# Kernel optimization log

Hardware: AMD Instinct MI355X
Metric: run time of the kernel (lower is better)

The kernel has to match this reference:

```python
import jax, jax.numpy as jnp
import numpy as np
import math

# ---- model constants (match init_kwargs) ----
B, T, HID = 2, 4096, 2048
H, D = 16, 128            # heads, head_dim; num_kv_heads == H
ROPE_DIM = 64             # head_dim * partial_rotary_factor (0.5)
THETA = 10000.0
EPS = 1e-6
CHUNK = 64                # chunk size for the chunked simple-GLA scan
LAYER_IDX, N_LAYERS = 12, 32


def _alibi_slopes(n):
    # power-of-2 path of build_slope_tensor
    start = 2.0 ** (-(2.0 ** -(math.log2(n) - 3.0)))
    return np.array([start ** (i + 1) for i in range(n)], dtype=np.float32)


def _layer_slope():
    scale = 1.0 - (LAYER_IDX - 1) / (N_LAYERS - 1) + 1e-5
    return jnp.asarray(-_alibi_slopes(H) * scale)  # [H], negative log-decay per step


def _rmsnorm(x, w):
    xf = x.astype(jnp.float32)
    var = jnp.mean(xf * xf, axis=-1, keepdims=True)
    return (w * (xf * jax.lax.rsqrt(var + EPS)).astype(x.dtype))


def _group_rmsnorm(x, w, groups):
    # x: [..., groups*gd]; normalize within each group, then elementwise weight
    shp = x.shape
    xg = x.reshape(shp[:-1] + (groups, shp[-1] // groups)).astype(jnp.float32)
    var = jnp.mean(xg * xg, axis=-1, keepdims=True)
    xn = (xg * jax.lax.rsqrt(var + EPS)).astype(x.dtype).reshape(shp)
    return w * xn


def _rope_cos_sin(position_ids):
    inv_freq = 1.0 / (THETA ** (jnp.arange(0, ROPE_DIM, 2, dtype=jnp.float32) / ROPE_DIM))
    freqs = position_ids.astype(jnp.float32)[..., None] * inv_freq  # [B,T,ROPE_DIM/2]
    emb = jnp.concatenate([freqs, freqs], axis=-1)                  # [B,T,ROPE_DIM]
    return jnp.cos(emb), jnp.sin(emb)


def _rotate_half(x):
    x1, x2 = jnp.split(x, 2, axis=-1)
    return jnp.concatenate([-x2, x1], axis=-1)


def _apply_rope(x, cos, sin):
    # x: [B,T,H,D]; partial rotary on first ROPE_DIM dims
    c = cos[:, :, None, :]
    s = sin[:, :, None, :]
    x_rot, x_pass = x[..., :ROPE_DIM], x[..., ROPE_DIM:]
    x_rot = x_rot * c + _rotate_half(x_rot) * s
    return jnp.concatenate([x_rot, x_pass], axis=-1)


def _chunk_simple_gla(q, k, v, slope):
    # q,k,v: [B,T,H,D]; slope: [H] (negative per-step log-decay)
    # recurrence: S_t = exp(slope)*S_{t-1} + k_t^T v_t ; o_t = q_t S_t
    q = q * (D ** -0.5)
    nc = T // CHUNK
    def to_chunks(x):
        # [B,T,H,D] -> [nc,B,H,CHUNK,D]
        return x.reshape(B, nc, CHUNK, H, D).transpose(1, 0, 3, 2, 4)
    qc, kc, vc = to_chunks(q), to_chunks(k), to_chunks(v)

    i = jnp.arange(CHUNK, dtype=jnp.float32)
    g = slope[:, None, None]                                  # [H,1,1]
    mask = jnp.where(i[:, None] >= i[None, :],
                     jnp.exp(g * (i[:, None] - i[None, :])), 0.0)   # [H,C,C]
    q_dec = jnp.exp(slope[:, None] * (i + 1.0))               # [H,C]
    k_dec = jnp.exp(slope[:, None] * (CHUNK - 1.0 - i))       # [H,C]
    ch_dec = jnp.exp(slope * CHUNK)                           # [H]

    S0 = jnp.zeros((B, H, D, D), q.dtype)

    def step(S, inp):
        qi, ki, vi = inp                                       # [B,H,C,D]
        att = jnp.einsum('bhcd,bhed->bhce', qi, ki) * mask[None]
        intra = jnp.einsum('bhce,bhed->bhcd', att, vi)
        inter = jnp.einsum('bhcd,bhde->bhce', qi * q_dec[None, :, :, None], S)
        S_new = ch_dec[None, :, None, None] * S + \
            jnp.einsum('bhcd,bhce->bhde', ki * k_dec[None, :, :, None], vi)
        return S_new, intra + inter

    _, o = jax.lax.scan(step, S0, (qc, kc, vc))                # o: [nc,B,H,C,D]
    return o.transpose(1, 0, 3, 2, 4).reshape(B, T, H * D)


def setup_inputs() -> dict:
    key = jax.random.key(0)
    ks = jax.random.split(key, 4)
    return {
        'hidden_states': jax.random.normal(ks[0], (B, T, HID), jnp.float32),
        'w_qkv': jax.random.normal(ks[1], (3 * H * D, HID), jnp.float32) * 0.02,
        'q_ln_w': jnp.ones((D,), jnp.float32),
        'k_ln_w': jnp.ones((D,), jnp.float32),
        'g_norm_w': jnp.ones((H * D,), jnp.float32),
        'w_g_proj': jax.random.normal(ks[2], (H * D, HID), jnp.float32) * 0.02,
        'w_dense': jax.random.normal(ks[3], (HID, H * D), jnp.float32) * 0.02,
        'position_ids': jnp.arange(B * T, dtype=jnp.int32).reshape(B, T) % T,
    }


def reference(hidden_states, w_qkv, q_ln_w, k_ln_w, g_norm_w, w_g_proj, w_dense, position_ids):
    slope = _layer_slope()
    qkv = jnp.einsum('bth,oh->bto', hidden_states, w_qkv)
    q, k, v = jnp.split(qkv, [H * D, 2 * H * D], axis=-1)
    q = q.reshape(B, T, H, D)
    k = k.reshape(B, T, H, D)
    v = v.reshape(B, T, H, D)
    # qk-norm (per-head RMSNorm)
    q = _rmsnorm(q, q_ln_w)
    k = _rmsnorm(k, k_ln_w)
    # partial RoPE
    cos, sin = _rope_cos_sin(position_ids)
    q = _apply_rope(q, cos, sin)
    k = _apply_rope(k, cos, sin)
    # chunked lightning (simple-GLA) linear attention
    o = _chunk_simple_gla(q, k, v, slope)                      # [B,T,H*D]
    # group RMSNorm (per head) + sigmoid output gate, then output proj
    gate = jax.nn.sigmoid(jnp.einsum('bth,oh->bto', hidden_states, w_g_proj))
    o = _group_rmsnorm(o, g_norm_w, groups=H) * gate
    return jnp.einsum('bto,ho->bth', o, w_dense)
```

## Files before the change

kernel.cpp:

```cpp
#include <hip/hip_runtime.h>
#include <math.h>

typedef short bf16x8 __attribute__((ext_vector_type(8)));
typedef float f32x4 __attribute__((ext_vector_type(4)));

#define LOG2E 1.4426950408889634f
#define GSCALE 0.6451712903225806f

__device__ __forceinline__ float bf2f(unsigned short h) {
    union { unsigned u; float f; } v; v.u = ((unsigned)h) << 16; return v.f;
}
__device__ __forceinline__ unsigned short f2bf(float f) {
    union { float f; unsigned u; } v; v.f = f;
    unsigned r = v.u + 0x7FFFu + ((v.u >> 16) & 1u);
    return (unsigned short)(r >> 16);
}

#define GLD16(lds, g)                                                          \
    __builtin_amdgcn_global_load_lds(                                          \
        (const __attribute__((address_space(1))) void*)(g),                    \
        (__attribute__((address_space(3))) void*)(lds), 16, 0, 0)

#define MFMA16(a, b, c) __builtin_amdgcn_mfma_f32_16x16x32_bf16(a, b, c, 0, 0, 0)

struct us4 { unsigned short a, b, c, d; };
__global__ __launch_bounds__(256) void cvt4_f32_bf16(
    const float* __restrict__ s0, const float* __restrict__ s1,
    const float* __restrict__ s2, const float* __restrict__ s3,
    unsigned short* __restrict__ dst, int c0, int c1, int c2, int n4)
{
    int i = blockIdx.x * 256 + threadIdx.x;
    if (i >= n4) return;
    const float* s; int off;
    if (i < c0)      { s = s0; off = i; }
    else if (i < c1) { s = s1; off = i - c0; }
    else if (i < c2) { s = s2; off = i - c1; }
    else             { s = s3; off = i - c2; }
    float4 v = ((const float4*)s)[off];
    us4 o = { f2bf(v.x), f2bf(v.y), f2bf(v.z), f2bf(v.w) };
    ((us4*)dst)[i] = o;
}

template <int EPI>
__global__ __launch_bounds__(512, 2) void gemm256(
    const unsigned short* __restrict__ A, const unsigned short* __restrict__ Bt,
    void* __restrict__ Cv,
    unsigned short* __restrict__ Qp, unsigned short* __restrict__ Kp,
    unsigned short* __restrict__ Vp, unsigned short* __restrict__ Gb,
    int M, int N, int K)
{
    __shared__ __attribute__((aligned(16))) unsigned short lA[2][16384];
    __shared__ __attribute__((aligned(16))) unsigned short lB[2][16384];

    const int tid  = threadIdx.x;
    const int lane = tid & 63, wave = tid >> 6;
    const int quad = lane >> 4, lr = lane & 15;
    const int wm   = (wave >> 2) * 128;
    const int wn   = (wave & 3) * 64;
    const int lsw  = lr & 7;

    const int nwg = (int)(gridDim.x * gridDim.y);
    const int lin = (int)(blockIdx.y * gridDim.x + blockIdx.x);
    const int swz = (lin & 7) * (nwg >> 3) + (lin >> 3);
    const int bn = swz % (int)gridDim.x, bm = swz / (int)gridDim.x;

    const unsigned short* Ab = A  + (long long)bm * 256 * K;
    const unsigned short* Bb = Bt + (long long)bn * 256 * K;

    const int c0r = tid, c1r = 512 + tid;
    const int row0 = c0r >> 3, row1 = c1r >> 3;
    const long long ga0 = (long long)row0 * K + ((c0r & 7) ^ (row0 & 7)) * 8;
    const long long ga1 = (long long)row1 * K + ((c1r & 7) ^ (row1 & 7)) * 8;
    const long long HK  = (long long)128 * K;
    const int l0 = c0r * 8, l1 = c1r * 8;

#define STAGE(ldsb, gb, half, kt)                                              \
    do {                                                                       \
        GLD16((ldsb) + (half) * 8192 + l0, (gb) + (half) * HK + (kt) + ga0);   \
        GLD16((ldsb) + (half) * 8192 + l1, (gb) + (half) * HK + (kt) + ga1);   \
    } while (0)

    f32x4 acc[8][4] = {};
    bf16x8 a[4][2], blo[2][2], bhi[2][2];

#define LOADA(buf, base)                                                       \
    _Pragma("unroll") for (int i = 0; i < 4; ++i)                              \
    _Pragma("unroll") for (int s = 0; s < 2; ++s)                              \
        a[i][s] = *(const bf16x8*)((buf) + ((base) + i * 16 + lr) * 64 +       \
                                   (((s * 4 + quad) ^ lsw) * 8));
#define LOADB(dst, buf, base)                                                  \
    _Pragma("unroll") for (int j = 0; j < 2; ++j)                              \
    _Pragma("unroll") for (int s = 0; s < 2; ++s)                              \
        dst[j][s] = *(const bf16x8*)((buf) + ((base) + j * 16 + lr) * 64 +     \
                                     (((s * 4 + quad) ^ lsw) * 8));
#define MFMAQ(MQ, NQ, BV)                                                      \
    _Pragma("unroll") for (int i = 0; i < 4; ++i)                              \
    _Pragma("unroll") for (int j = 0; j < 2; ++j)                              \
    _Pragma("unroll") for (int s = 0; s < 2; ++s)                              \
        acc[(MQ) * 4 + i][(NQ) * 2 + j] =                                      \
            MFMA16(a[i][s], BV[j][s], acc[(MQ) * 4 + i][(NQ) * 2 + j]);

#define BARR()  asm volatile("s_barrier" ::: "memory")
#define LGKM0() asm volatile("s_waitcnt lgkmcnt(0)" ::: "memory")
#define VM6()   asm volatile("s_waitcnt vmcnt(6)" ::: "memory")
#define PTAIL() do { BARR(); LGKM0(); __builtin_amdgcn_sched_barrier(0);       \
                     __builtin_amdgcn_s_setprio(1); } while (0)
#define PEND()  do { __builtin_amdgcn_s_setprio(0); BARR(); } while (0)

    STAGE(lA[0], Ab, 0, 0); STAGE(lA[0], Ab, 1, 0);
    STAGE(lB[0], Bb, 0, 0); STAGE(lB[0], Bb, 1, 0);
    STAGE(lB[1], Bb, 0, 64); STAGE(lB[1], Bb, 1, 64);
    STAGE(lA[1], Ab, 0, 64);
    VM6();
    BARR();

    const int NT = K >> 6;
    for (int it = 0; it < (NT >> 1); ++it) {
        const int v   = 2 * it + 1;
        const int kn0 = (2 * it + 2 < NT) ? (2 * it + 2) * 64 : 0;
        const int kn1 = (2 * it + 3 < NT) ? (2 * it + 3) * 64 : 0;
        LOADA(lA[0], wm); LOADB(blo, lB[0], wn);
        STAGE(lA[1], Ab, 1, v * 64);
        PTAIL(); MFMAQ(0, 0, blo); PEND();
        LOADB(bhi, lB[0], wn + 32);
        PTAIL(); MFMAQ(0, 1, bhi); PEND();
        LOADA(lA[0], wm + 64);
        STAGE(lB[0], Bb, 0, kn0);
        PTAIL(); MFMAQ(1, 1, bhi); PEND();
        STAGE(lB[0], Bb, 1, kn0); STAGE(lA[0], Ab, 0, kn0);
        VM6(); BARR();
        __builtin_amdgcn_s_setprio(1); MFMAQ(1, 0, blo); PEND();
        LOADA(lA[1], wm); LOADB(blo, lB[1], wn);
        STAGE(lA[0], Ab, 1, kn0);
        PTAIL(); MFMAQ(0, 0, blo); PEND();
        LOADB(bhi, lB[1], wn + 32);
        PTAIL(); MFMAQ(0, 1, bhi); PEND();
        LOADA(lA[1], wm + 64);
        STAGE(lB[1], Bb, 0, kn1);
        PTAIL(); MFMAQ(1, 1, bhi); PEND();
        STAGE(lB[1], Bb, 1, kn1); STAGE(lA[1], Ab, 0, kn1);
        VM6(); BARR();
        __builtin_amdgcn_s_setprio(1); MFMAQ(1, 0, blo); PEND();
    }
    asm volatile("s_waitcnt vmcnt(0)" ::: "memory");

#pragma unroll
    for (int i = 0; i < 8; ++i)
#pragma unroll
        for (int j = 0; j < 4; ++j)
#pragma unroll
            for (int r = 0; r < 4; ++r) {
                int row = bm * 256 + wm + i * 16 + quad * 4 + r;
                int col = bn * 256 + wn + j * 16 + lr;
                float vv = acc[i][j][r];
                if (EPI == 0) {
                    if (col < 6144) {
                        int tens = col >> 11, h = (col >> 7) & 15, e = col & 127;
                        int b = row >> 12, t = row & 4095;
                        long long dst = (((long long)(b * 16 + h)) * 4096 + t) * 128 + e;
                        unsigned short* P = (tens == 0) ? Qp : ((tens == 1) ? Kp : Vp);
                        P[dst] = f2bf(vv);
                    } else {
                        vv = 1.0f / (1.0f + __expf(-vv));
                        Gb[(long long)row * 2048 + (col - 6144)] = f2bf(vv);
                    }
                } else {
                    ((float*)Cv)[(long long)row * N + col] = vv;
                }
            }
#undef STAGE
#undef LOADA
#undef LOADB
#undef MFMAQ
#undef BARR
#undef LGKM0
#undef VM6
#undef PTAIL
#undef PEND
}

__global__ __launch_bounds__(256) void norm_rope(
    unsigned short* __restrict__ Qp, unsigned short* __restrict__ Kp,
    const float* __restrict__ qw, const float* __restrict__ kw,
    const int* __restrict__ pos_ids)
{
    const int bid  = blockIdx.x;
    const int tg   = bid & 1023, h = (bid >> 10) & 15, b = bid >> 14;
    const int wave = threadIdx.x >> 6, lane = threadIdx.x & 63;
    const int t    = tg * 4 + wave;
    const long long rowbase = (((long long)(b * 16 + h)) * 4096 + t) * 128;
    const int pos = pos_ids[b * 4096 + t];
    const int d0  = lane * 2;

    float c0 = 1.f, s0 = 0.f, c1 = 1.f, s1 = 0.f;
    if (lane < 32) {
        float fj0 = (float)(d0 & 31), fj1 = (float)((d0 + 1) & 31);
        float if0 = exp2f(-fj0 * 0.4152410118609203f);
        float if1 = exp2f(-fj1 * 0.4152410118609203f);
        sincosf((float)pos * if0, &s0, &c0);
        sincosf((float)pos * if1, &s1, &c1);
    }
    const float w0q = qw[d0], w1q = qw[d0 + 1];
    const float w0k = kw[d0], w1k = kw[d0 + 1];

#pragma unroll
    for (int which = 0; which < 2; ++which) {
        unsigned short* P = which ? Kp : Qp;
        float w0 = which ? w0k : w0q, w1 = which ? w1k : w1q;
        unsigned u = *(const unsigned*)(P + rowbase + d0);
        float x0 = bf2f(u & 0xFFFF), x1 = bf2f(u >> 16);
        float ss = x0 * x0 + x1 * x1;
#pragma unroll
        for (int off = 32; off; off >>= 1) ss += __shfl_xor(ss, off);
        float r  = rsqrtf(ss * (1.0f / 128.0f) + 1e-6f);
        float xn0 = x0 * r * w0;
        float xn1 = x1 * r * w1;
        float p0 = __shfl_xor(xn0, 16);
        float p1 = __shfl_xor(xn1, 16);
        float y0, y1;
        if (d0 < 32)      { y0 = xn0 * c0 - p0 * s0; y1 = xn1 * c1 - p1 * s1; }
        else if (d0 < 64) { y0 = xn0 * c0 + p0 * s0; y1 = xn1 * c1 + p1 * s1; }
        else              { y0 = xn0; y1 = xn1; }
        if (which == 0) { y0 *= 0.08838834764831845f; y1 *= 0.08838834764831845f; }
        *(unsigned*)(P + rowbase + d0) =
            (unsigned)f2bf(y0) | ((unsigned)f2bf(y1) << 16);
    }
}

__global__ __launch_bounds__(256) void gla_chunk(
    const unsigned short* __restrict__ Qp, const unsigned short* __restrict__ Kp,
    const unsigned short* __restrict__ Vp,
    unsigned short* __restrict__ Oint, unsigned short* __restrict__ Ubuf)
{
    __shared__ __attribute__((aligned(16))) unsigned short sK[64 * 136];
    __shared__ __attribute__((aligned(16))) unsigned short sVT[128 * 72];
    __shared__ __attribute__((aligned(16))) unsigned short sKT[128 * 72];
    __shared__ __attribute__((aligned(16))) unsigned short sAtt[64 * 72];

    const int bid = blockIdx.x;
    const int n = bid & 63, h = (bid >> 6) & 15, b = bid >> 10;
    const int tid = threadIdx.x, wave = tid >> 6, lane = tid & 63;
    const int quad = lane >> 4, lr = lane & 15;
    const float gl2 = -exp2f(-0.5f * (float)(h + 1)) * GSCALE * LOG2E;

    const long long rb = (((long long)(b * 16 + h)) * 4096 + (long long)n * 64) * 128;

    const int cS = wave * 16 + lr;
    const float qsc = exp2f(gl2 * (float)cS);
    bf16x8 qf[4];
#pragma unroll
    for (int ks = 0; ks < 4; ++ks) {
        union { uint4 v; unsigned short s[8]; } in, ou;
        in.v = *(const uint4*)(Qp + rb + cS * 128 + ks * 32 + quad * 8);
#pragma unroll
        for (int j = 0; j < 8; ++j) ou.s[j] = f2bf(bf2f(in.s[j]) * qsc);
        qf[ks] = *(bf16x8*)&ou;
    }
#pragma unroll
    for (int rr = 0; rr < 4; ++rr) {
        int idx = rr * 256 + tid;
        int c = idx >> 4, d8 = (idx & 15) << 3;
        *(uint4*)(sK + c * 136 + d8) = *(const uint4*)(Kp + rb + c * 128 + d8);
    }
#pragma unroll
    for (int rr = 0; rr < 4; ++rr) {
        int idx = rr * 256 + tid;
        int c = idx & 63, g8 = (idx >> 6) << 3;
        union { uint4 v; unsigned short s[8]; } vv, kk;
        vv.v = *(const uint4*)(Vp + rb + c * 128 + g8);
        kk.v = *(const uint4*)(Kp + rb + c * 128 + g8);
        float kdsc = exp2f(gl2 * (float)(64 - c));
#pragma unroll
        for (int j = 0; j < 8; ++j) {
            sVT[(g8 + j) * 72 + c] = vv.s[j];
            sKT[(g8 + j) * 72 + c] = f2bf(bf2f(kk.s[j]) * kdsc);
        }
    }
    __syncthreads();

    f32x4 aacc[4] = {};
#pragma unroll
    for (int nj = 0; nj < 4; ++nj)
#pragma unroll
        for (int ks = 0; ks < 4; ++ks) {
            bf16x8 bf = *(const bf16x8*)(sK + (nj * 16 + lr) * 136 + ks * 32 + quad * 8);
            aacc[nj] = MFMA16(qf[ks], bf, aacc[nj]);
        }
#pragma unroll
    for (int nj = 0; nj < 4; ++nj) {
        int c2 = nj * 16 + lr;
        float colf = exp2f(-gl2 * (float)c2);
#pragma unroll
        for (int r = 0; r < 4; ++r) {
            int c = wave * 16 + quad * 4 + r;
            sAtt[c * 72 + c2] = f2bf((c >= c2) ? aacc[nj][r] * colf : 0.0f);
        }
    }
    f32x4 Sacc[2][8] = {};
#pragma unroll
    for (int me = 0; me < 2; ++me)
#pragma unroll
        for (int ks = 0; ks < 2; ++ks) {
            bf16x8 af = *(const bf16x8*)(sVT + (wave * 32 + me * 16 + lr) * 72 + ks * 32 + quad * 8);
#pragma unroll
            for (int dj = 0; dj < 8; ++dj) {
                bf16x8 bf = *(const bf16x8*)(sKT + (dj * 16 + lr) * 72 + ks * 32 + quad * 8);
                Sacc[me][dj] = MFMA16(af, bf, Sacc[me][dj]);
            }
        }
    const long long ub = ((long long)((b * 16 + h) * 64 + n)) * 16384;
#pragma unroll
    for (int me = 0; me < 2; ++me)
#pragma unroll
        for (int r = 0; r < 4; ++r) {
            int e = wave * 32 + me * 16 + quad * 4 + r;
#pragma unroll
            for (int dj = 0; dj < 8; ++dj)
                Ubuf[ub + e * 128 + dj * 16 + lr] = f2bf(Sacc[me][dj][r]);
        }
    __syncthreads();

    f32x4 oacc[8] = {};
#pragma unroll
    for (int ks = 0; ks < 2; ++ks) {
        bf16x8 af = *(const bf16x8*)(sAtt + cS * 72 + ks * 32 + quad * 8);
#pragma unroll
        for (int ej = 0; ej < 8; ++ej) {
            bf16x8 bf = *(const bf16x8*)(sVT + (ej * 16 + lr) * 72 + ks * 32 + quad * 8);
            oacc[ej] = MFMA16(af, bf, oacc[ej]);
        }
    }
#pragma unroll
    for (int ej = 0; ej < 8; ++ej)
#pragma unroll
        for (int r = 0; r < 4; ++r) {
            int c = wave * 16 + quad * 4 + r;
            long long off = ((long long)(b * 4096 + n * 64 + c)) * 2048 + h * 128 + ej * 16 + lr;
            Oint[off] = f2bf(oacc[ej][r]);
        }
}

__global__ __launch_bounds__(256) void gla_scan(
    const unsigned short* __restrict__ Ubuf, unsigned short* __restrict__ STbuf)
{
    const int bid = blockIdx.x;
    const int es = bid & 7, bh = bid >> 3;
    const int h = bh & 15;
    const float gl2 = -exp2f(-0.5f * (float)(h + 1)) * GSCALE * LOG2E;
    const float chd = exp2f(gl2 * 64.0f);
    const int tid = threadIdx.x;
    const long long base = (long long)bh * 64 * 16384 + es * 2048 + tid * 8;
    float st[8] = {};
    for (int n = 0; n < 64; ++n) {
        long long a = base + (long long)n * 16384;
        union { uint4 v; unsigned short s[8]; } u, o;
        u.v = *(const uint4*)(Ubuf + a);
#pragma unroll
        for (int j = 0; j < 8; ++j) o.s[j] = f2bf(st[j]);
        *(uint4*)(STbuf + a) = o.v;
#pragma unroll
        for (int j = 0; j < 8; ++j) st[j] = st[j] * chd + bf2f(u.s[j]);
    }
}

__global__ __launch_bounds__(256) void gla_inter(
    const unsigned short* __restrict__ Qp, const unsigned short* __restrict__ STbuf,
    unsigned short* __restrict__ Ob, const unsigned short* __restrict__ Gb,
    const float* __restrict__ W)
{
    __shared__ __attribute__((aligned(16))) unsigned short sST[128 * 136];
    const int bid = blockIdx.x;
    const int n = bid & 63, h = (bid >> 6) & 15, b = bid >> 10;
    const int tid = threadIdx.x, wave = tid >> 6, lane = tid & 63;
    const int quad = lane >> 4, lr = lane & 15;
    const float gl2 = -exp2f(-0.5f * (float)(h + 1)) * GSCALE * LOG2E;
    const long long rb = (((long long)(b * 16 + h)) * 4096 + (long long)n * 64) * 128;
    const long long stb = ((long long)((b * 16 + h) * 64 + n)) * 16384;

#pragma unroll
    for (int rr = 0; rr < 8; ++rr) {
        int idx = rr * 256 + tid;
        int row = idx >> 4, d8 = (idx & 15) << 3;
        *(uint4*)(sST + row * 136 + d8) = *(const uint4*)(STbuf + stb + row * 128 + d8);
    }
    const int cS = wave * 16 + lr;
    const float qsc = exp2f(gl2 * (float)cS);
    bf16x8 qf[4];
#pragma unroll
    for (int ks = 0; ks < 4; ++ks) {
        union { uint4 v; unsigned short s[8]; } in, ou;
        in.v = *(const uint4*)(Qp + rb + cS * 128 + ks * 32 + quad * 8);
#pragma unroll
        for (int j = 0; j < 8; ++j) ou.s[j] = f2bf(bf2f(in.s[j]) * qsc);
        qf[ks] = *(bf16x8*)&ou;
    }
    __syncthreads();

    f32x4 oacc[8] = {};
#pragma unroll
    for (int ks = 0; ks < 4; ++ks)
#pragma unroll
        for (int ej = 0; ej < 8; ++ej) {
            bf16x8 bf = *(const bf16x8*)(sST + (ej * 16 + lr) * 136 + ks * 32 + quad * 8);
            oacc[ej] = MFMA16(qf[ks], bf, oacc[ej]);
        }

    float w[8];
#pragma unroll
    for (int ej = 0; ej < 8; ++ej) w[ej] = W[h * 128 + ej * 16 + lr];

    float ss[4] = {};
#pragma unroll
    for (int r = 0; r < 4; ++r) {
        int c = wave * 16 + quad * 4 + r;
        long long off = ((long long)(b * 4096 + n * 64 + c)) * 2048 + h * 128;
#pragma unroll
        for (int ej = 0; ej < 8; ++ej) {
            float v = oacc[ej][r] + bf2f(Ob[off + ej * 16 + lr]);
            oacc[ej][r] = v;
            ss[r] += v * v;
        }
    }
#pragma unroll
    for (int r = 0; r < 4; ++r) {
#pragma unroll
        for (int o2 = 1; o2 < 16; o2 <<= 1) ss[r] += __shfl_xor(ss[r], o2);
        float rn = rsqrtf(ss[r] * (1.0f / 128.0f) + 1e-6f);
        int c = wave * 16 + quad * 4 + r;
        long long off = ((long long)(b * 4096 + n * 64 + c)) * 2048 + h * 128;
#pragma unroll
        for (int ej = 0; ej < 8; ++ej) {
            float g = bf2f(Gb[off + ej * 16 + lr]);
            Ob[off + ej * 16 + lr] = f2bf(oacc[ej][r] * rn * w[ej] * g);
        }
    }
}

extern "C" void kernel_launch(void* const* d_in, const int* in_sizes, int n_in,
                              void* d_out, int out_size, void* d_ws, size_t ws_size,
                              hipStream_t stream)
{
    const float* hid   = (const float*)d_in[0];
    const float* w_qkv = (const float*)d_in[1];
    const float* q_ln  = (const float*)d_in[2];
    const float* k_ln  = (const float*)d_in[3];
    const float* g_nw  = (const float*)d_in[4];
    const float* w_g   = (const float*)d_in[5];
    const float* w_d   = (const float*)d_in[6];
    const int*   pos   = (const int*)d_in[7];

    const size_t PLANE = (size_t)2 * 16 * 4096 * 128;
    unsigned short* Qp    = (unsigned short*)d_ws;
    unsigned short* Kp    = Qp + PLANE;
    unsigned short* Vp    = Kp + PLANE;
    unsigned short* Ob    = Vp + PLANE;
    unsigned short* Gb    = Ob + PLANE;
    unsigned short* hidb  = Gb + PLANE;
    unsigned short* wqkvb = hidb + (size_t)8192 * 2048;
    unsigned short* wgb   = wqkvb + (size_t)6144 * 2048;
    unsigned short* wdb   = wgb + (size_t)2048 * 2048;
    unsigned short* Ubuf  = hidb;
    unsigned short* STbuf = Kp;

    dim3 blk(256);
    const int c0 = 8192 * 2048 / 4;
    const int c1 = c0 + 6144 * 2048 / 4;
    const int c2 = c1 + 2048 * 2048 / 4;
    const int n4 = c2 + 2048 * 2048 / 4;
    cvt4_f32_bf16<<<(n4 + 255) / 256, blk, 0, stream>>>(
        hid, w_qkv, w_g, w_d, hidb, c0, c1, c2, n4);

    gemm256<0><<<dim3(32, 32), dim3(512), 0, stream>>>(
        hidb, wqkvb, nullptr, Qp, Kp, Vp, Gb, 8192, 8192, 2048);
    norm_rope<<<32768, blk, 0, stream>>>(Qp, Kp, q_ln, k_ln, pos);
    gla_chunk<<<2048, blk, 0, stream>>>(Qp, Kp, Vp, Ob, Ubuf);
    gla_scan<<<256, blk, 0, stream>>>(Ubuf, STbuf);
    gla_inter<<<2048, blk, 0, stream>>>(Qp, STbuf, Ob, Gb, g_nw);
    gemm256<2><<<dim3(8, 32), dim3(512), 0, stream>>>(
        Ob, wdb, d_out, nullptr, nullptr, nullptr, nullptr, 8192, 2048, 2048);
}
```

Baseline: 656.0 us.

## Remap GEMM workgroups per XCD by row and rebalance async load staging

Changes the workgroup-to-tile mapping so each XCD owns a contiguous band of M-tile rows and walks N tiles, which is meant to improve L2 reuse of A rows within an XCD. It also redistributes the global-to-LDS stage issues across the MFMA phases, adding a vmcnt(4) wait in the first half-iteration and adding sched barriers before lowering priority. Together these aim to smooth memory issue and cut stalls. The new mapping assumes gridDim.y is divisible by 8, and the changed wait counts must still match the outstanding loads.

```diff
diff --git a/kernel.cpp b/kernel.cpp
--- a/kernel.cpp
+++ b/kernel.cpp
@@ -59,10 +59,11 @@
     const int wn   = (wave & 3) * 64;
     const int lsw  = lr & 7;
 
-    const int nwg = (int)(gridDim.x * gridDim.y);
     const int lin = (int)(blockIdx.y * gridDim.x + blockIdx.x);
-    const int swz = (lin & 7) * (nwg >> 3) + (lin >> 3);
-    const int bn = swz % (int)gridDim.x, bm = swz / (int)gridDim.x;
+    const int xcd = lin & 7, j = lin >> 3;
+    const int RPC = (int)gridDim.y >> 3;
+    const int bm  = xcd * RPC + (j % RPC);
+    const int bn  = j / RPC;
 
     const unsigned short* Ab = A  + (long long)bm * 256 * K;
     const unsigned short* Bb = Bt + (long long)bn * 256 * K;
@@ -89,23 +90,27 @@
         a[i][s] = *(const bf16x8*)((buf) + ((base) + i * 16 + lr) * 64 +       \
                                    (((s * 4 + quad) ^ lsw) * 8));
 #define LOADB(dst, buf, base)                                                  \
-    _Pragma("unroll") for (int j = 0; j < 2; ++j)                              \
+    _Pragma("unroll") for (int j2 = 0; j2 < 2; ++j2)                           \
     _Pragma("unroll") for (int s = 0; s < 2; ++s)                              \
-        dst[j][s] = *(const bf16x8*)((buf) + ((base) + j * 16 + lr) * 64 +     \
-                                     (((s * 4 + quad) ^ lsw) * 8));
+        dst[j2][s] = *(const bf16x8*)((buf) + ((base) + j2 * 16 + lr) * 64 +   \
+                                      (((s * 4 + quad) ^ lsw) * 8));
 #define MFMAQ(MQ, NQ, BV)                                                      \
     _Pragma("unroll") for (int i = 0; i < 4; ++i)                              \
-    _Pragma("unroll") for (int j = 0; j < 2; ++j)                              \
+    _Pragma("unroll") for (int j2 = 0; j2 < 2; ++j2)                           \
     _Pragma("unroll") for (int s = 0; s < 2; ++s)                              \
-        acc[(MQ) * 4 + i][(NQ) * 2 + j] =                                      \
-            MFMA16(a[i][s], BV[j][s], acc[(MQ) * 4 + i][(NQ) * 2 + j]);
+        acc[(MQ) * 4 + i][(NQ) * 2 + j2] =                                     \
+            MFMA16(a[i][s], BV[j2][s], acc[(MQ) * 4 + i][(NQ) * 2 + j2]);
 
 #define BARR()  asm volatile("s_barrier" ::: "memory")
 #define LGKM0() asm volatile("s_waitcnt lgkmcnt(0)" ::: "memory")
+#define VM4()   asm volatile("s_waitcnt vmcnt(4)" ::: "memory")
 #define VM6()   asm volatile("s_waitcnt vmcnt(6)" ::: "memory")
-#define PTAIL() do { BARR(); LGKM0(); __builtin_amdgcn_sched_barrier(0);       \
+#define SBAR()  __builtin_amdgcn_sched_barrier(0)
+#define PBEG()  do { BARR(); LGKM0(); SBAR();                                  \
                      __builtin_amdgcn_s_setprio(1); } while (0)
-#define PEND()  do { __builtin_amdgcn_s_setprio(0); BARR(); } while (0)
+#define PBEGW(W) do { W(); BARR(); SBAR();                                     \
+                     __builtin_amdgcn_s_setprio(1); } while (0)
+#define PEND()  do { SBAR(); __builtin_amdgcn_s_setprio(0); BARR(); } while (0)
 
     STAGE(lA[0], Ab, 0, 0); STAGE(lA[0], Ab, 1, 0);
     STAGE(lB[0], Bb, 0, 0); STAGE(lB[0], Bb, 1, 0);
@@ -121,38 +126,37 @@
         const int kn1 = (2 * it + 3 < NT) ? (2 * it + 3) * 64 : 0;
         LOADA(lA[0], wm); LOADB(blo, lB[0], wn);
         STAGE(lA[1], Ab, 1, v * 64);
-        PTAIL(); MFMAQ(0, 0, blo); PEND();
+        PBEG(); MFMAQ(0, 0, blo); PEND();
         LOADB(bhi, lB[0], wn + 32);
-        PTAIL(); MFMAQ(0, 1, bhi); PEND();
+        PBEG(); MFMAQ(0, 1, bhi); PEND();
         LOADA(lA[0], wm + 64);
         STAGE(lB[0], Bb, 0, kn0);
-        PTAIL(); MFMAQ(1, 1, bhi); PEND();
-        STAGE(lB[0], Bb, 1, kn0); STAGE(lA[0], Ab, 0, kn0);
-        VM6(); BARR();
-        __builtin_amdgcn_s_setprio(1); MFMAQ(1, 0, blo); PEND();
+        PBEG(); MFMAQ(1, 1, bhi); PEND();
+        STAGE(lB[0], Bb, 1, kn0);
+        PBEGW(VM4); MFMAQ(1, 0, blo); PEND();
         LOADA(lA[1], wm); LOADB(blo, lB[1], wn);
+        STAGE(lA[0], Ab, 0, kn0);
+        PBEG(); MFMAQ(0, 0, blo); PEND();
+        LOADB(bhi, lB[1], wn + 32);
         STAGE(lA[0], Ab, 1, kn0);
-        PTAIL(); MFMAQ(0, 0, blo); PEND();
-        LOADB(bhi, lB[1], wn + 32);
-        PTAIL(); MFMAQ(0, 1, bhi); PEND();
+        PBEG(); MFMAQ(0, 1, bhi); PEND();
         LOADA(lA[1], wm + 64);
         STAGE(lB[1], Bb, 0, kn1);
-        PTAIL(); MFMAQ(1, 1, bhi); PEND();
+        PBEG(); MFMAQ(1, 1, bhi); PEND();
         STAGE(lB[1], Bb, 1, kn1); STAGE(lA[1], Ab, 0, kn1);
-        VM6(); BARR();
-        __builtin_amdgcn_s_setprio(1); MFMAQ(1, 0, blo); PEND();
+        PBEGW(VM6); MFMAQ(1, 0, blo); PEND();
     }
     asm volatile("s_waitcnt vmcnt(0)" ::: "memory");
 
 #pragma unroll
     for (int i = 0; i < 8; ++i)
 #pragma unroll
-        for (int j = 0; j < 4; ++j)
+        for (int j2 = 0; j2 < 4; ++j2)
 #pragma unroll
             for (int r = 0; r < 4; ++r) {
                 int row = bm * 256 + wm + i * 16 + quad * 4 + r;
-                int col = bn * 256 + wn + j * 16 + lr;
-                float vv = acc[i][j][r];
+                int col = bn * 256 + wn + j2 * 16 + lr;
+                float vv = acc[i][j2][r];
                 if (EPI == 0) {
                     if (col < 6144) {
                         int tens = col >> 11, h = (col >> 7) & 15, e = col & 127;
@@ -174,8 +178,11 @@
 #undef MFMAQ
 #undef BARR
 #undef LGKM0
+#undef VM4
 #undef VM6
-#undef PTAIL
+#undef SBAR
+#undef PBEG
+#undef PBEGW
 #undef PEND
 }
 
```

New measurement: 634.9 us. -3.2%, faster.
